# Performance work log

Measured on AMD Instinct MI355X. Metric: run time of the kernel, lower is better.

The kernel has to match this reference:

```python
import jax, jax.numpy as jnp
import numpy as np

N, C, H, W = 32, 24, 14, 14
HD, GH, AS = 128, 256, 28
D_IN = (C + 2) * 2 + HD  # 180


def setup_inputs() -> dict:
    key = jax.random.key(0)
    ks = jax.random.split(key, 10)
    s = 0.05
    inp = {
        "x": jax.random.normal(ks[0], (N, C, H, W), jnp.float32),
        "code": jax.random.normal(ks[1], (N, HD), jnp.float32),
        "gw0": jax.random.normal(ks[2], (D_IN, GH), jnp.float32) * s,
        "gb0": jnp.zeros((GH,), jnp.float32),
        "gw1": jax.random.normal(ks[3], (GH, GH), jnp.float32) * s,
        "gb1": jnp.zeros((GH,), jnp.float32),
        "gw2": jax.random.normal(ks[4], (GH, GH), jnp.float32) * s,
        "gb2": jnp.zeros((GH,), jnp.float32),
        "gw3": jax.random.normal(ks[5], (GH, GH), jnp.float32) * s,
        "gb3": jnp.zeros((GH,), jnp.float32),
        "fw0": jax.random.normal(ks[6], (GH, GH), jnp.float32) * s,
        "fb0": jnp.zeros((GH,), jnp.float32),
        "fw1": jax.random.normal(ks[7], (GH, GH), jnp.float32) * s,
        "fb1": jnp.zeros((GH,), jnp.float32),
        "fw2": jax.random.normal(ks[8], (GH, AS), jnp.float32) * s,
        "fb2": jnp.zeros((AS,), jnp.float32),
    }
    return inp


def _rn_encode(x, code):
    n, c, h, w = x.shape
    o = h * w
    hd = code.shape[1]
    # coordinates: torch.linspace(-h/2, h/2, h) over row dim, (-w/2, w/2, w) over col dim
    xs = jnp.linspace(-h / 2.0, h / 2.0, h, dtype=jnp.float32)
    ys = jnp.linspace(-w / 2.0, w / 2.0, w, dtype=jnp.float32)
    coord = jnp.stack(
        [jnp.broadcast_to(xs[:, None], (h, w)).reshape(o),
         jnp.broadcast_to(ys[None, :], (h, w)).reshape(o)], axis=-1)  # (o, 2)
    feats = x.reshape(n, c, o).transpose(0, 2, 1)  # (n, o, c)
    feats = jnp.concatenate([feats, jnp.broadcast_to(coord, (n, o, 2))], axis=-1)  # (n, o, c+2)
    # pairs[n, i, j] = [feats[n, j], feats[n, i], code[n]]  (matches torch expand semantics)
    p1 = jnp.broadcast_to(feats[:, None, :, :], (n, o, o, c + 2))
    p2 = jnp.broadcast_to(feats[:, :, None, :], (n, o, o, c + 2))
    q = jnp.broadcast_to(code[:, None, None, :], (n, o, o, hd))
    return jnp.concatenate([p1, p2, q], axis=-1).reshape(n, o * o, -1)


def reference(x, code, gw0, gb0, gw1, gb1, gw2, gb2, gw3, gb3,
              fw0, fb0, fw1, fb1, fw2, fb2):
    pairs = _rn_encode(x, code)  # (n, o^2, 180)
    h1 = jax.nn.relu(pairs @ gw0 + gb0)
    h1 = jax.nn.relu(h1 @ gw1 + gb1)
    h1 = jax.nn.relu(h1 @ gw2 + gb2)
    h1 = jax.nn.relu(h1 @ gw3 + gb3)
    relations = h1.sum(axis=1)  # (n, GH) sum-pool over all pairs
    r = jax.nn.relu(relations @ fw0 + fb0)
    r = jax.nn.relu(r @ fw1 + fb1)
    logits = r @ fw2 + fb2  # last layer linear (last=True)
    return logits
```

## Files before the change

### kernel.cpp

```cpp
#include <hip/hip_runtime.h>


typedef __attribute__((ext_vector_type(8))) short short8;
typedef __attribute__((ext_vector_type(4))) float f32x4;

#define NIMG 32
#define O 196
#define GH 256
#define AS 28
#define ROWS 112
#define CHUNKS 343
#define LDH 264

static __device__ __forceinline__ unsigned short f2bf(float f) {
    union { float f; unsigned int u; } v; v.f = f;
    unsigned int r = v.u + 0x7FFFu + ((v.u >> 16) & 1u);
    return (unsigned short)(r >> 16);
}

__global__ void k_ajbi(const float* __restrict__ x, const float* __restrict__ gw0,
                       float* __restrict__ AJ, float* __restrict__ BI) {
    const int np = blockIdx.x;
    const int n = np / O, p = np - n * O;
    const int g = threadIdx.x;
    __shared__ float fs[26];
    if (g < 24)       fs[g]  = x[(n * 24 + g) * O + p];
    else if (g == 24) fs[24] = -7.0f + (float)(p / 14) * (14.0f / 13.0f);
    else if (g == 25) fs[25] = -7.0f + (float)(p % 14) * (14.0f / 13.0f);
    __syncthreads();
    float aj = 0.f, bi = 0.f;
#pragma unroll
    for (int c = 0; c < 26; ++c) {
        const float f = fs[c];
        aj = fmaf(f, gw0[c * GH + g], aj);
        bi = fmaf(f, gw0[(26 + c) * GH + g], bi);
    }
    AJ[np * GH + g] = aj;
    BI[np * GH + g] = bi;
}

__global__ void k_cc(const float* __restrict__ code, const float* __restrict__ gw0,
                     const float* __restrict__ gb0, float* __restrict__ CC) {
    const int n = blockIdx.x, g = threadIdx.x;
    __shared__ float cs[128];
    if (g < 128) cs[g] = code[n * 128 + g];
    __syncthreads();
    float acc = gb0[g];
    for (int k = 0; k < 128; ++k) acc = fmaf(cs[k], gw0[(52 + k) * GH + g], acc);
    CC[n * GH + g] = acc;
}

__global__ void k_pack(const float* __restrict__ gw1, const float* __restrict__ gw2,
                       const float* __restrict__ gw3, unsigned short* __restrict__ pW) {
    const int idx = blockIdx.x * 256 + threadIdx.x;
    const int L = idx >> 16;
    const int rem = idx & 0xFFFF;
    const int e = rem & 7;
    const int lane = (rem >> 3) & 63;
    const int ks = (rem >> 9) & 7;
    const int ntile = rem >> 12;
    const int k = ks * 32 + ((lane >> 4) << 3) + e;
    const int col = ntile * 16 + (lane & 15);
    const float* W = (L == 0) ? gw1 : (L == 1) ? gw2 : gw3;
    pW[idx] = f2bf(W[k * GH + col]);
}

__global__ __launch_bounds__(256, 2) void k_main(
    const float* __restrict__ AJ, const float* __restrict__ BI,
    const float* __restrict__ CC, const unsigned short* __restrict__ pW,
    const float* __restrict__ gb1, const float* __restrict__ gb2,
    const float* __restrict__ gb3, float* __restrict__ rel) {
    __shared__ __attribute__((aligned(16))) unsigned short h[ROWS * LDH];

    const int blk = blockIdx.x;
    const int n = blk / CHUNKS;
    const int chunk = blk - n * CHUNKS;
    const int row_base = chunk * ROWS;
    const int t = threadIdx.x;
    const int wave = t >> 6;
    const int lane = t & 63;
    const int l15 = lane & 15;
    const int q = lane >> 4;

    {
        const float cc = CC[n * GH + t];
        int i = row_base / O;
        int j = row_base - i * O;
        const float* ajb = AJ + (n * O) * GH + t;
        const float* bib = BI + (n * O) * GH + t;
        for (int e = 0; e < ROWS; ++e) {
            float v = ajb[j * GH] + bib[i * GH] + cc;
            h[e * LDH + t] = f2bf(fmaxf(v, 0.0f));
            if (++j == O) { j = 0; ++i; }
        }
    }
    __syncthreads();

    const float* gbs[3] = {gb1, gb2, gb3};
    for (int layer = 0; layer < 3; ++layer) {
        f32x4 acc[7][4];
#pragma unroll
        for (int mt = 0; mt < 7; ++mt)
#pragma unroll
            for (int nt = 0; nt < 4; ++nt) acc[mt][nt] = (f32x4){0.f, 0.f, 0.f, 0.f};

        const short8* wp = (const short8*)(pW + layer * 65536);
        const int lds_base = l15 * LDH + q * 8;
#pragma unroll 2
        for (int ks = 0; ks < 8; ++ks) {
            short8 b[4];
#pragma unroll
            for (int nt = 0; nt < 4; ++nt)
                b[nt] = wp[((wave * 4 + nt) * 8 + ks) * 64 + lane];
            short8 a[7];
#pragma unroll
            for (int mt = 0; mt < 7; ++mt)
                a[mt] = *(const short8*)&h[mt * 16 * LDH + lds_base + ks * 32];
#pragma unroll
            for (int mt = 0; mt < 7; ++mt)
#pragma unroll
                for (int nt = 0; nt < 4; ++nt)
                    acc[mt][nt] = __builtin_amdgcn_mfma_f32_16x16x32_bf16(
                        a[mt], b[nt], acc[mt][nt], 0, 0, 0);
        }
        __syncthreads();

        const float* gb = gbs[layer];
        if (layer < 2) {
#pragma unroll
            for (int nt = 0; nt < 4; ++nt) {
                const int col = wave * 64 + nt * 16 + l15;
                const float bias = gb[col];
#pragma unroll
                for (int mt = 0; mt < 7; ++mt) {
#pragma unroll
                    for (int r = 0; r < 4; ++r) {
                        const int row = mt * 16 + q * 4 + r;
                        h[row * LDH + col] = f2bf(fmaxf(acc[mt][nt][r] + bias, 0.0f));
                    }
                }
            }
            __syncthreads();
        } else {
#pragma unroll
            for (int nt = 0; nt < 4; ++nt) {
                const int col = wave * 64 + nt * 16 + l15;
                const float bias = gb[col];
                float s = 0.f;
#pragma unroll
                for (int mt = 0; mt < 7; ++mt)
#pragma unroll
                    for (int r = 0; r < 4; ++r)
                        s += fmaxf(acc[mt][nt][r] + bias, 0.0f);
                s += __shfl_xor(s, 16);
                s += __shfl_xor(s, 32);
                if (q == 0) atomicAdd(&rel[n * GH + col], s);
            }
        }
    }
}

__global__ void k_fmlp(const float* __restrict__ rel,
                       const float* __restrict__ fw0, const float* __restrict__ fb0,
                       const float* __restrict__ fw1, const float* __restrict__ fb1,
                       const float* __restrict__ fw2, const float* __restrict__ fb2,
                       float* __restrict__ out) {
    __shared__ float b0[GH], b1[GH];
    const int n = blockIdx.x, g = threadIdx.x;
    b0[g] = rel[n * GH + g];
    __syncthreads();
    float a = fb0[g];
    for (int k = 0; k < GH; ++k) a = fmaf(b0[k], fw0[k * GH + g], a);
    b1[g] = fmaxf(a, 0.f);
    __syncthreads();
    float c = fb1[g];
    for (int k = 0; k < GH; ++k) c = fmaf(b1[k], fw1[k * GH + g], c);
    b0[g] = fmaxf(c, 0.f);
    __syncthreads();
    if (g < AS) {
        float o = fb2[g];
        for (int k = 0; k < GH; ++k) o = fmaf(b0[k], fw2[k * AS + g], o);
        out[n * AS + g] = o;
    }
}

extern "C" void kernel_launch(void* const* d_in, const int* in_sizes, int n_in,
                              void* d_out, int out_size, void* d_ws, size_t ws_size,
                              hipStream_t stream) {
    const float* x    = (const float*)d_in[0];
    const float* code = (const float*)d_in[1];
    const float* gw0  = (const float*)d_in[2];
    const float* gb0  = (const float*)d_in[3];
    const float* gw1  = (const float*)d_in[4];
    const float* gb1  = (const float*)d_in[5];
    const float* gw2  = (const float*)d_in[6];
    const float* gb2  = (const float*)d_in[7];
    const float* gw3  = (const float*)d_in[8];
    const float* gb3  = (const float*)d_in[9];
    const float* fw0  = (const float*)d_in[10];
    const float* fb0  = (const float*)d_in[11];
    const float* fw1  = (const float*)d_in[12];
    const float* fb1  = (const float*)d_in[13];
    const float* fw2  = (const float*)d_in[14];
    const float* fb2  = (const float*)d_in[15];
    float* out = (float*)d_out;

    char* ws = (char*)d_ws;
    float*          AJ  = (float*)(ws + 0);
    float*          BI  = (float*)(ws + 6422528);
    float*          CC  = (float*)(ws + 12845056);
    float*          rel = (float*)(ws + 12877824);
    unsigned short* pW  = (unsigned short*)(ws + 12910592);

    hipMemsetAsync(rel, 0, NIMG * GH * sizeof(float), stream);
    k_ajbi<<<NIMG * O, 256, 0, stream>>>(x, gw0, AJ, BI);
    k_cc<<<NIMG, 256, 0, stream>>>(code, gw0, gb0, CC);
    k_pack<<<3 * 256, 256, 0, stream>>>(gw1, gw2, gw3, pW);
    k_main<<<NIMG * CHUNKS, 256, 0, stream>>>(AJ, BI, CC, pW, gb1, gb2, gb3, rel);
    k_fmlp<<<NIMG, 256, 0, stream>>>(rel, fw0, fb0, fw1, fb1, fw2, fb2, out);
}
```

Baseline: 653.3 us.

## Use 512-thread 128-row tiles with XOR-swizzled LDS and vectorized first-layer fill

```diff
diff --git a/kernel.cpp b/kernel.cpp
--- a/kernel.cpp
+++ b/kernel.cpp
@@ -1,4 +1,5 @@
 #include <hip/hip_runtime.h>
+#include <hip/hip_bf16.h>
 
 
 typedef __attribute__((ext_vector_type(8))) short short8;
@@ -6,19 +7,30 @@
 
 #define NIMG 32
 #define O 196
+#define PAIRS 38416
 #define GH 256
 #define AS 28
-#define ROWS 112
-#define CHUNKS 343
-#define LDH 264
+#define ROWS 128
+#define CHUNKS 301
 
 static __device__ __forceinline__ unsigned short f2bf(float f) {
-    union { float f; unsigned int u; } v; v.f = f;
-    unsigned int r = v.u + 0x7FFFu + ((v.u >> 16) & 1u);
-    return (unsigned short)(r >> 16);
+    __hip_bfloat16 h = __float2bfloat16(f);
+    return *reinterpret_cast<unsigned short*>(&h);
+}
+
+__global__ void k_cc(const float* __restrict__ code, const float* __restrict__ gw0,
+                     const float* __restrict__ gb0, float* __restrict__ CC) {
+    const int n = blockIdx.x, g = threadIdx.x;
+    __shared__ float cs[128];
+    if (g < 128) cs[g] = code[n * 128 + g];
+    __syncthreads();
+    float acc = gb0[g];
+    for (int k = 0; k < 128; ++k) acc = fmaf(cs[k], gw0[(52 + k) * GH + g], acc);
+    CC[n * GH + g] = acc;
 }
 
 __global__ void k_ajbi(const float* __restrict__ x, const float* __restrict__ gw0,
+                       const float* __restrict__ CC,
                        float* __restrict__ AJ, float* __restrict__ BI) {
     const int np = blockIdx.x;
     const int n = np / O, p = np - n * O;
@@ -28,7 +40,7 @@
     else if (g == 24) fs[24] = -7.0f + (float)(p / 14) * (14.0f / 13.0f);
     else if (g == 25) fs[25] = -7.0f + (float)(p % 14) * (14.0f / 13.0f);
     __syncthreads();
-    float aj = 0.f, bi = 0.f;
+    float aj = CC[n * GH + g], bi = 0.f;
 #pragma unroll
     for (int c = 0; c < 26; ++c) {
         const float f = fs[c];
@@ -37,17 +49,6 @@
     }
     AJ[np * GH + g] = aj;
     BI[np * GH + g] = bi;
-}
-
-__global__ void k_cc(const float* __restrict__ code, const float* __restrict__ gw0,
-                     const float* __restrict__ gb0, float* __restrict__ CC) {
-    const int n = blockIdx.x, g = threadIdx.x;
-    __shared__ float cs[128];
-    if (g < 128) cs[g] = code[n * 128 + g];
-    __syncthreads();
-    float acc = gb0[g];
-    for (int k = 0; k < 128; ++k) acc = fmaf(cs[k], gw0[(52 + k) * GH + g], acc);
-    CC[n * GH + g] = acc;
 }
 
 __global__ void k_pack(const float* __restrict__ gw1, const float* __restrict__ gw2,
@@ -65,12 +66,12 @@
     pW[idx] = f2bf(W[k * GH + col]);
 }
 
-__global__ __launch_bounds__(256, 2) void k_main(
+__global__ __launch_bounds__(512, 4) void k_main(
     const float* __restrict__ AJ, const float* __restrict__ BI,
-    const float* __restrict__ CC, const unsigned short* __restrict__ pW,
+    const unsigned short* __restrict__ pW,
     const float* __restrict__ gb1, const float* __restrict__ gb2,
     const float* __restrict__ gb3, float* __restrict__ rel) {
-    __shared__ __attribute__((aligned(16))) unsigned short h[ROWS * LDH];
+    __shared__ __attribute__((aligned(16))) unsigned short h[ROWS * GH];
 
     const int blk = blockIdx.x;
     const int n = blk / CHUNKS;
@@ -81,43 +82,60 @@
     const int lane = t & 63;
     const int l15 = lane & 15;
     const int q = lane >> 4;
+    const int mh = wave >> 2;
+    const int wq = wave & 3;
+    const bool tail = (chunk == CHUNKS - 1);
 
     {
-        const float cc = CC[n * GH + t];
-        int i = row_base / O;
-        int j = row_base - i * O;
-        const float* ajb = AJ + (n * O) * GH + t;
-        const float* bib = BI + (n * O) * GH + t;
-        for (int e = 0; e < ROWS; ++e) {
-            float v = ajb[j * GH] + bib[i * GH] + cc;
-            h[e * LDH + t] = f2bf(fmaxf(v, 0.0f));
-            if (++j == O) { j = 0; ++i; }
+        const int i0 = row_base / O;
+        const int j00 = row_base - i0 * O;
+        const int i1 = min(i0 + 1, O - 1);
+        const float4 bi0 = *(const float4*)&BI[(n * O + i0) * GH + lane * 4];
+        const float4 bi1 = *(const float4*)&BI[(n * O + i1) * GH + lane * 4];
+        for (int e = 0; e < 16; ++e) {
+            const int r = wave + e * 8;
+            const int jj = j00 + r;
+            const bool wrap = (jj >= O);
+            const int j = wrap ? jj - O : jj;
+            const float4 aj = *(const float4*)&AJ[(n * O + j) * GH + lane * 4];
+            const float4 bi = wrap ? bi1 : bi0;
+            const unsigned int lo = (unsigned)f2bf(fmaxf(aj.x + bi.x, 0.f)) |
+                                    ((unsigned)f2bf(fmaxf(aj.y + bi.y, 0.f)) << 16);
+            const unsigned int hi = (unsigned)f2bf(fmaxf(aj.z + bi.z, 0.f)) |
+                                    ((unsigned)f2bf(fmaxf(aj.w + bi.w, 0.f)) << 16);
+            const int byteoff = r * 512 + ((lane * 8) ^ ((r & 7) << 4));
+            uint2 dd; dd.x = lo; dd.y = hi;
+            *(uint2*)((char*)h + byteoff) = dd;
         }
     }
     __syncthreads();
 
     const float* gbs[3] = {gb1, gb2, gb3};
+    const int X = (l15 & 7) << 4;
+    const char* hb = (const char*)h + (mh * 64 + l15) * 512;
+    const int cb2 = (wq * 64 + l15) * 2;
+
     for (int layer = 0; layer < 3; ++layer) {
-        f32x4 acc[7][4];
-#pragma unroll
-        for (int mt = 0; mt < 7; ++mt)
+        f32x4 acc[4][4];
+#pragma unroll
+        for (int mt = 0; mt < 4; ++mt)
 #pragma unroll
             for (int nt = 0; nt < 4; ++nt) acc[mt][nt] = (f32x4){0.f, 0.f, 0.f, 0.f};
 
         const short8* wp = (const short8*)(pW + layer * 65536);
-        const int lds_base = l15 * LDH + q * 8;
-#pragma unroll 2
+#pragma unroll 1
         for (int ks = 0; ks < 8; ++ks) {
             short8 b[4];
 #pragma unroll
             for (int nt = 0; nt < 4; ++nt)
-                b[nt] = wp[((wave * 4 + nt) * 8 + ks) * 64 + lane];
-            short8 a[7];
-#pragma unroll
-            for (int mt = 0; mt < 7; ++mt)
-                a[mt] = *(const short8*)&h[mt * 16 * LDH + lds_base + ks * 32];
-#pragma unroll
-            for (int mt = 0; mt < 7; ++mt)
+                b[nt] = wp[((wq * 4 + nt) * 8 + ks) * 64 + lane];
+            const int off = (ks * 64 + q * 16) ^ X;
+            short8 a[4];
+#pragma unroll
+            for (int mt = 0; mt < 4; ++mt)
+                a[mt] = *(const short8*)(hb + off + mt * 8192);
+#pragma unroll
+            for (int mt = 0; mt < 4; ++mt)
 #pragma unroll
                 for (int nt = 0; nt < 4; ++nt)
                     acc[mt][nt] = __builtin_amdgcn_mfma_f32_16x16x32_bf16(
@@ -129,29 +147,32 @@
         if (layer < 2) {
 #pragma unroll
             for (int nt = 0; nt < 4; ++nt) {
-                const int col = wave * 64 + nt * 16 + l15;
-                const float bias = gb[col];
-#pragma unroll
-                for (int mt = 0; mt < 7; ++mt) {
-#pragma unroll
-                    for (int r = 0; r < 4; ++r) {
-                        const int row = mt * 16 + q * 4 + r;
-                        h[row * LDH + col] = f2bf(fmaxf(acc[mt][nt][r] + bias, 0.0f));
-                    }
+                const float bias = gb[wq * 64 + nt * 16 + l15];
+#pragma unroll
+                for (int r = 0; r < 4; ++r) {
+                    const int rowl = q * 4 + r;
+                    const int base = (((mh * 64 + rowl) * 512) + cb2 + nt * 32)
+                                     ^ ((rowl & 7) << 4);
+#pragma unroll
+                    for (int mt = 0; mt < 4; ++mt)
+                        *(unsigned short*)((char*)h + base + mt * 8192) =
+                            f2bf(fmaxf(acc[mt][nt][r] + bias, 0.0f));
                 }
             }
             __syncthreads();
         } else {
 #pragma unroll
             for (int nt = 0; nt < 4; ++nt) {
-                const int col = wave * 64 + nt * 16 + l15;
+                const int col = wq * 64 + nt * 16 + l15;
                 const float bias = gb[col];
                 float s = 0.f;
 #pragma unroll
-                for (int mt = 0; mt < 7; ++mt)
+                for (int mt = 0; mt < 4; ++mt) {
+                    if (tail && !(mh == 0 && mt == 0)) continue;
 #pragma unroll
                     for (int r = 0; r < 4; ++r)
                         s += fmaxf(acc[mt][nt][r] + bias, 0.0f);
+                }
                 s += __shfl_xor(s, 16);
                 s += __shfl_xor(s, 32);
                 if (q == 0) atomicAdd(&rel[n * GH + col], s);
@@ -213,9 +234,9 @@
     unsigned short* pW  = (unsigned short*)(ws + 12910592);
 
     hipMemsetAsync(rel, 0, NIMG * GH * sizeof(float), stream);
-    k_ajbi<<<NIMG * O, 256, 0, stream>>>(x, gw0, AJ, BI);
     k_cc<<<NIMG, 256, 0, stream>>>(code, gw0, gb0, CC);
+    k_ajbi<<<NIMG * O, 256, 0, stream>>>(x, gw0, CC, AJ, BI);
     k_pack<<<3 * 256, 256, 0, stream>>>(gw1, gw2, gw3, pW);
-    k_main<<<NIMG * CHUNKS, 256, 0, stream>>>(AJ, BI, CC, pW, gb1, gb2, gb3, rel);
+    k_main<<<NIMG * CHUNKS, 512, 0, stream>>>(AJ, BI, pW, gb1, gb2, gb3, rel);
     k_fmlp<<<NIMG, 256, 0, stream>>>(rel, fw0, fb0, fw1, fb1, fw2, fb2, out);
 }
```

New measurement: 525.5 us. 19.6% less time.
